# Optimization experiments

Hardware: AMD Instinct MI355X
Metric: run time of the kernel (lower is better)

## Reference

```python
import jax, jax.numpy as jnp
import numpy as np

N, E = 20000, 640000
F_IN, H, T = 64, 256, 64  # in_channels = T, edge_attr dim = T -> EdgeConv MLP in = 3*T


def _lin(key, fan_in, fan_out):
    k1, k2 = jax.random.split(key)
    s = 1.0 / np.sqrt(fan_in)
    W = jax.random.uniform(k1, (fan_in, fan_out), jnp.float32, -s, s)
    b = jax.random.uniform(k2, (fan_out,), jnp.float32, -s, s)
    return W, b


def setup_inputs() -> dict:
    key = jax.random.key(0)
    ks = jax.random.split(key, 12)
    x = jax.random.normal(ks[0], (N, F_IN), jnp.float32)
    edge_index = jax.random.randint(ks[1], (2, E), 0, N, jnp.int32)
    edge_attr = jax.random.normal(ks[2], (E, T), jnp.float32)
    conv1_W, conv1_b = _lin(ks[3], F_IN, H)
    e_W1, e_b1 = _lin(ks[4], 3 * T, H)
    e_W2, e_b2 = _lin(ks[5], H, H)
    conv2_W, conv2_b = _lin(ks[6], 2 * H, H)
    conv3_W, conv3_b = _lin(ks[7], H, F_IN)
    lin1_W, lin1_b = _lin(ks[8], 2 * F_IN, F_IN)
    lin2_W, lin2_b = _lin(ks[9], F_IN, 128)
    lin3_W, lin3_b = _lin(ks[10], 128, 32)
    lin4_W, lin4_b = _lin(ks[11], 32, 2)
    return dict(x=x, edge_index=edge_index, edge_attr=edge_attr,
                conv1_W=conv1_W, conv1_b=conv1_b,
                e_W1=e_W1, e_b1=e_b1, e_W2=e_W2, e_b2=e_b2,
                conv2_W=conv2_W, conv2_b=conv2_b,
                conv3_W=conv3_W, conv3_b=conv3_b,
                lin1_W=lin1_W, lin1_b=lin1_b, lin2_W=lin2_W, lin2_b=lin2_b,
                lin3_W=lin3_W, lin3_b=lin3_b, lin4_W=lin4_W, lin4_b=lin4_b)


def reference(x, edge_index, edge_attr,
              conv1_W, conv1_b, e_W1, e_b1, e_W2, e_b2,
              conv2_W, conv2_b, conv3_W, conv3_b,
              lin1_W, lin1_b, lin2_W, lin2_b, lin3_W, lin3_b, lin4_W, lin4_b):
    n = x.shape[0]
    src, dst = edge_index[0], edge_index[1]
    # GCN symmetric norm with self-loops (deg counted on dst, +1 for self-loop)
    deg = jax.ops.segment_sum(jnp.ones_like(src, jnp.float32), dst, num_segments=n) + 1.0
    dis = jax.lax.rsqrt(deg)

    def gcn(h, W, b):
        hw = h @ W
        msg = hw[src] * (dis[src] * dis[dst])[:, None]
        # self-loop contribution: norm = dis[i]^2
        return jax.ops.segment_sum(msg, dst, num_segments=n) + hw * (dis * dis)[:, None] + b

    out1 = jax.nn.relu(gcn(x, conv1_W, conv1_b))
    # EdgeConv: MLP(cat[x_i, x_j, edge_attr]) with max aggregation onto dst (x_i = target)
    m = jnp.concatenate([x[dst], x[src], edge_attr], axis=1)      # [E, 3T]
    m = jax.nn.relu(m @ e_W1 + e_b1) @ e_W2 + e_b2                 # [E, H]
    agg = jax.ops.segment_max(m, dst, num_segments=n)
    agg = jnp.where(jnp.isfinite(agg), agg, 0.0)                   # nodes with no in-edges
    out_e1 = jax.nn.relu(agg)

    out2 = jax.nn.relu(gcn(jnp.concatenate([out1, out_e1], axis=1), conv2_W, conv2_b))
    out3 = jax.nn.relu(gcn(out2, conv3_W, conv3_b))
    h = jnp.concatenate([x, out3], axis=1)
    h = jax.nn.softplus(h @ lin1_W + lin1_b)
    h = jax.nn.softplus(h @ lin2_W + lin2_b)
    h = jax.nn.softplus(h @ lin3_W + lin3_b)
    h = h @ lin4_W + lin4_b                                        # [N, 2]
    return (h[:, 0], h[:, 1])
```

## Files before the change

kernel.cpp:

```cpp
#include <hip/hip_runtime.h>
#include <stdint.h>

typedef __bf16 bf16x8 __attribute__((ext_vector_type(8)));
typedef float f32x4 __attribute__((ext_vector_type(4)));
typedef unsigned short u16x8 __attribute__((ext_vector_type(8)));
typedef unsigned long long ull_t;
typedef unsigned short ushort_t;

#define DEV __device__ __forceinline__

DEV unsigned short f2bf(float f) {
  __bf16 b = (__bf16)f;
  return __builtin_bit_cast(unsigned short, b);
}

DEV float bf2f(unsigned short b) { return __uint_as_float((unsigned int)b << 16); }

DEV f32x4 zero4() { f32x4 z = {0.f, 0.f, 0.f, 0.f}; return z; }

DEV float softplusf(float v) { return (v > 15.f) ? v : log1pf(expf(v)); }

__global__ void pack_weight(const float* __restrict__ W, unsigned short* __restrict__ P,
                            int K, int Ncols, int permk) {
  int idx = blockIdx.x * 256 + threadIdx.x;
  if (idx >= K * Ncols) return;
  int j = idx & 7;
  int lane = (idx >> 3) & 63;
  int rest = idx >> 9;
  int NT = Ncols >> 4;
  int nt = rest % NT;
  int kt = rest / NT;
  int k = kt * 32 + ((j >> 2) * 16) + ((lane >> 4) * 4) + (j & 3);
  if (permk) k = (k & ~63) | ((k & 3) << 4) | ((k >> 2) & 15);
  int col = nt * 16 + (lane & 15);
  P[idx] = f2bf(W[(size_t)k * Ncols + col]);
}

__global__ void k_deg(const int* __restrict__ dst, int* __restrict__ degi, int E) {
  int i = blockIdx.x * 256 + threadIdx.x;
  if (i < E) atomicAdd(&degi[dst[i]], 1);
}

__global__ void k_dis(const int* __restrict__ degi, float* __restrict__ dis, int n) {
  int i = blockIdx.x * 256 + threadIdx.x;
  if (i < n) dis[i] = rsqrtf((float)degi[i] + 1.0f);
}

__global__ __launch_bounds__(1024) void k_scan(const int* __restrict__ degi,
                                               int* __restrict__ ptr, int n) {
  __shared__ int part[1024];
  const int tid = threadIdx.x;
  const int chunk = (n + 1023) / 1024;
  const int b = tid * chunk;
  const int e2 = min(n, b + chunk);
  int s = 0;
  for (int i = b; i < e2; ++i) s += degi[i];
  part[tid] = s;
  __syncthreads();
  for (int off = 1; off < 1024; off <<= 1) {
    int val = (tid >= off) ? part[tid - off] : 0;
    __syncthreads();
    part[tid] += val;
    __syncthreads();
  }
  int run = (tid == 0) ? 0 : part[tid - 1];
  for (int i = b; i < e2; ++i) {
    ptr[i] = run;
    run += degi[i];
  }
  if (tid == 1023) ptr[n] = run;
}

__global__ void k_fill(const int* __restrict__ srcs, const int* __restrict__ dsts,
                       const int* __restrict__ ptr, const float* __restrict__ dis,
                       int* __restrict__ fillc,
                       int2* __restrict__ sc_s, int* __restrict__ dst_s,
                       int* __restrict__ perm_s, int E) {
  int e = blockIdx.x * 256 + threadIdx.x;
  if (e >= E) return;
  int d = dsts[e];
  int s = srcs[e];
  int pos = ptr[d] + atomicAdd(&fillc[d], 1);
  float c = dis[s] * dis[d];
  sc_s[pos] = make_int2(s, __float_as_int(c));
  dst_s[pos] = d;
  perm_s[pos] = e;
}

template <int COLS, bool FINALIZE, bool INBF16>
__global__ __launch_bounds__(256) void k_gather_agg(
    const void* __restrict__ featv, const int2* __restrict__ sc,
    const int* __restrict__ ptr, const float* __restrict__ dis,
    const void* __restrict__ hwv, const float* __restrict__ bias,
    float* __restrict__ out, int n) {
  constexpr int V = COLS / 64;
  const int v = blockIdx.x * 4 + (threadIdx.x >> 6);
  if (v >= n) return;
  const int lane = threadIdx.x & 63;
  const int beg = ptr[v], end = ptr[v + 1];

  auto loadrow = [&](int s, float* f) {
    if constexpr (INBF16) {
      const ushort_t* feat = (const ushort_t*)featv;
      if constexpr (V == 4) {
        ushort4 u = *(const ushort4*)(feat + (size_t)s * COLS + lane * 4);
        f[0] = bf2f(u.x); f[1] = bf2f(u.y); f[2] = bf2f(u.z); f[3] = bf2f(u.w);
      } else {
        f[0] = bf2f(feat[(size_t)s * COLS + lane]);
      }
    } else {
      const float* feat = (const float*)featv;
      if constexpr (V == 4) {
        float4 q = *(const float4*)(feat + (size_t)s * COLS + lane * 4);
        f[0] = q.x; f[1] = q.y; f[2] = q.z; f[3] = q.w;
      } else {
        f[0] = feat[(size_t)s * COLS + lane];
      }
    }
  };

  float acc[V];
#pragma unroll
  for (int i = 0; i < V; ++i) acc[i] = 0.f;
  const int cnt = end - beg;
  const int2* scp = sc + beg;
  int i = 0;
  for (; i + 4 <= cnt; i += 4) {
    int2 s0 = scp[i], s1 = scp[i + 1], s2 = scp[i + 2], s3 = scp[i + 3];
    float f0[V], f1[V], f2[V], f3[V];
    loadrow(s0.x, f0); loadrow(s1.x, f1); loadrow(s2.x, f2); loadrow(s3.x, f3);
    float c0 = __int_as_float(s0.y), c1 = __int_as_float(s1.y);
    float c2 = __int_as_float(s2.y), c3 = __int_as_float(s3.y);
#pragma unroll
    for (int j = 0; j < V; ++j)
      acc[j] += f0[j] * c0 + f1[j] * c1 + f2[j] * c2 + f3[j] * c3;
  }
  for (; i < cnt; ++i) {
    int2 s0 = scp[i];
    float c0 = __int_as_float(s0.y);
    float f0[V];
    loadrow(s0.x, f0);
#pragma unroll
    for (int j = 0; j < V; ++j) acc[j] += f0[j] * c0;
  }
  float* op = out + (size_t)v * COLS + lane * V;
  if constexpr (FINALIZE) {
    const float dv = dis[v];
    float d2 = dv * dv;
    float h[V];
    if constexpr (INBF16) {
      const ushort_t* hw = (const ushort_t*)hwv;
      if constexpr (V == 4) {
        ushort4 u = *(const ushort4*)(hw + (size_t)v * COLS + lane * 4);
        h[0] = bf2f(u.x); h[1] = bf2f(u.y); h[2] = bf2f(u.z); h[3] = bf2f(u.w);
      } else {
        h[0] = bf2f(hw[(size_t)v * COLS + lane]);
      }
    } else {
      const float* hw = (const float*)hwv;
      if constexpr (V == 4) {
        float4 q = *(const float4*)(hw + (size_t)v * COLS + lane * 4);
        h[0] = q.x; h[1] = q.y; h[2] = q.z; h[3] = q.w;
      } else {
        h[0] = hw[(size_t)v * COLS + lane];
      }
    }
#pragma unroll
    for (int i2 = 0; i2 < V; ++i2)
      acc[i2] = fmaxf(acc[i2] + h[i2] * d2 + bias[lane * V + i2], 0.f);
  }
  if constexpr (V == 4) {
    *(float4*)op = make_float4(acc[0], acc[1], acc[2], acc[3]);
  } else {
    op[0] = acc[0];
  }
}

template <int K, int NOUT, bool COMPOSE, bool RELUBIAS, bool OUTBF16>
__global__ __launch_bounds__(256, 2) void gcn_gemm(
    const float* __restrict__ inA, const float* __restrict__ inB,
    const float* __restrict__ dis,
    const unsigned short* __restrict__ Wp, const float* __restrict__ bias,
    void* __restrict__ outv, int out_stride, int nrows) {
  constexpr int NT = NOUT / 16;
  constexpr int NTW = NOUT / 64;
  __shared__ unsigned short s_in[64 * K];
  const int tid = threadIdx.x;
  const int r0 = blockIdx.x * 64;

  constexpr int C4R = K / 4;
  for (int idx = tid; idx < 64 * C4R; idx += 256) {
    int row = idx / C4R;
    int rem = idx - row * C4R;
    int grow = r0 + row;
    float4 v = make_float4(0.f, 0.f, 0.f, 0.f);
    if (grow < nrows) {
      v = *(const float4*)&inA[(size_t)grow * K + rem * 4];
      if constexpr (COMPOSE) {
        float d = dis[grow];
        d *= d;
        float4 w2 = *(const float4*)&inB[(size_t)grow * K + rem * 4];
        v.x += w2.x * d; v.y += w2.y * d; v.z += w2.z * d; v.w += w2.w * d;
      }
    }
    ushort4 b;
    b.x = f2bf(v.x); b.y = f2bf(v.y); b.z = f2bf(v.z); b.w = f2bf(v.w);
    *(ushort4*)&s_in[row * K + ((rem ^ (row & 7)) * 4)] = b;
  }
  __syncthreads();

  const int lane = tid & 63, wid = tid >> 6;
  const int lr = lane & 15, lg = lane >> 4;
  f32x4 acc[4][NTW];
#pragma unroll
  for (int m = 0; m < 4; ++m)
#pragma unroll
    for (int n2 = 0; n2 < NTW; ++n2) acc[m][n2] = zero4();

#pragma unroll
  for (int kt = 0; kt < K / 32; ++kt) {
    bf16x8 a[4];
#pragma unroll
    for (int m = 0; m < 4; ++m) {
      int rA = m * 16 + lr;
      int c1 = (kt * 8 + lg) ^ (rA & 7);
      int c2 = (kt * 8 + lg + 4) ^ (rA & 7);
      union { bf16x8 v; ull_t q[2]; } u;
      u.q[0] = *(const ull_t*)&s_in[rA * K + c1 * 4];
      u.q[1] = *(const ull_t*)&s_in[rA * K + c2 * 4];
      a[m] = u.v;
    }
#pragma unroll
    for (int n2 = 0; n2 < NTW; ++n2) {
      int nt = wid * NTW + n2;
      bf16x8 b = *(const bf16x8*)&Wp[(((kt * NT + nt) * 64 + lane) * 8)];
#pragma unroll
      for (int m = 0; m < 4; ++m)
        acc[m][n2] = __builtin_amdgcn_mfma_f32_16x16x32_bf16(a[m], b, acc[m][n2], 0, 0, 0);
    }
  }

#pragma unroll
  for (int n2 = 0; n2 < NTW; ++n2) {
    int col = (wid * NTW + n2) * 16 + lr;
    float bv = 0.f;
    if (RELUBIAS) bv = bias[col];
#pragma unroll
    for (int m = 0; m < 4; ++m) {
#pragma unroll
      for (int r = 0; r < 4; ++r) {
        int grow = r0 + m * 16 + lg * 4 + r;
        if (grow < nrows) {
          float v = acc[m][n2][r];
          if (RELUBIAS) v = fmaxf(v + bv, 0.f);
          if constexpr (OUTBF16) {
            ((ushort_t*)outv)[(size_t)grow * out_stride + col] = f2bf(v);
          } else {
            ((float*)outv)[(size_t)grow * out_stride + col] = v;
          }
        }
      }
    }
  }
}

__global__ __launch_bounds__(512, 4) void k_edgeconv(
    const float* __restrict__ x, const float* __restrict__ ea,
    const int2* __restrict__ sc_s, const int* __restrict__ dst_s,
    const int* __restrict__ perm_s,
    const unsigned short* __restrict__ W1p, const float* __restrict__ b1,
    const unsigned short* __restrict__ W2p, const float* __restrict__ b2,
    float* __restrict__ h2, int E) {
  __shared__ unsigned short s_buf[256 * 72];
  __shared__ int s_src[64], s_dst[64], s_perm[64];
  __shared__ ull_t s_mask;
  const int tid = threadIdx.x;
  const int e0 = blockIdx.x * 64;
  const int lane = tid & 63, wid = tid >> 6;
  if (tid < 64) {
    int e = e0 + tid;
    s_src[tid] = (e < E) ? sc_s[e].x : 0;
    s_dst[tid] = (e < E) ? dst_s[e] : 0;
    s_perm[tid] = (e < E) ? perm_s[e] : 0;
  }
  __syncthreads();
  if (wid == 0) {
    bool chg = (lane > 0) && (s_dst[lane] != s_dst[lane - 1]);
    ull_t m = __ballot(chg);
    if (lane == 0) s_mask = m;
  }
#pragma unroll
  for (int seg = 0; seg < 3; ++seg) {
#pragma unroll
    for (int it = 0; it < 2; ++it) {
      int idx = it * 512 + tid;
      int ei = idx >> 4;
      int q = idx & 15;
      const float* row;
      if (seg == 0) row = x + (unsigned)s_dst[ei] * 64u;
      else if (seg == 1) row = x + (unsigned)s_src[ei] * 64u;
      else row = ea + (unsigned)s_perm[ei] * 64u;
      float4 v = make_float4(0.f, 0.f, 0.f, 0.f);
      if (e0 + ei < E) v = *(const float4*)(row + q * 4);
      ushort4 b;
      b.x = f2bf(v.x); b.y = f2bf(v.y); b.z = f2bf(v.z); b.w = f2bf(v.w);
      int chunk = (seg * 16 + q) ^ (ei & 7);
      *(ushort4*)&s_buf[ei * 192 + chunk * 4] = b;
    }
  }

  const int wr = wid >> 2;
  const int wc = wid & 3;
  const int lr = lane & 15, lg = lane >> 4;

  bf16x8 bn1[4];
#pragma unroll
  for (int n2 = 0; n2 < 4; ++n2)
    bn1[n2] = *(const bf16x8*)&W1p[(((0 * 16 + wc * 4 + n2) * 64 + lane) * 8)];

  __syncthreads();

  f32x4 acc[2][4];
#pragma unroll
  for (int m = 0; m < 2; ++m)
#pragma unroll
    for (int n2 = 0; n2 < 4; ++n2) acc[m][n2] = zero4();

#pragma unroll
  for (int kt = 0; kt < 6; ++kt) {
    bf16x8 bc[4];
#pragma unroll
    for (int n2 = 0; n2 < 4; ++n2) bc[n2] = bn1[n2];
    if (kt < 5) {
#pragma unroll
      for (int n2 = 0; n2 < 4; ++n2)
        bn1[n2] = *(const bf16x8*)&W1p[((((kt + 1) * 16 + wc * 4 + n2) * 64 + lane) * 8)];
    }
    bf16x8 a[2];
#pragma unroll
    for (int m = 0; m < 2; ++m) {
      int rA = wr * 32 + m * 16 + lr;
      int rr = rA & 7;
      union { bf16x8 v; ull_t q[2]; } u;
      u.q[0] = *(const ull_t*)&s_buf[rA * 192 + ((kt * 8 + lg) ^ rr) * 4];
      u.q[1] = *(const ull_t*)&s_buf[rA * 192 + ((kt * 8 + lg + 4) ^ rr) * 4];
      a[m] = u.v;
    }
#pragma unroll
    for (int n2 = 0; n2 < 4; ++n2)
#pragma unroll
      for (int m = 0; m < 2; ++m)
        acc[m][n2] = __builtin_amdgcn_mfma_f32_16x16x32_bf16(a[m], bc[n2], acc[m][n2], 0, 0, 0);
  }

  bf16x8 bn2[4];
#pragma unroll
  for (int n2 = 0; n2 < 4; ++n2)
    bn2[n2] = *(const bf16x8*)&W2p[(((0 * 16 + wc * 4 + n2) * 64 + lane) * 8)];

  __syncthreads();

  {
    float b1v[4];
#pragma unroll
    for (int n2 = 0; n2 < 4; ++n2) b1v[n2] = b1[(wc * 4 + n2) * 16 + lr];
#pragma unroll
    for (int m = 0; m < 2; ++m) {
#pragma unroll
      for (int r = 0; r < 4; ++r) {
        int row = wr * 32 + m * 16 + lg * 4 + r;
        union { ushort_t h[4]; ull_t q; } pk;
        pk.h[0] = f2bf(fmaxf(acc[m][0][r] + b1v[0], 0.f));
        pk.h[1] = f2bf(fmaxf(acc[m][1][r] + b1v[1], 0.f));
        pk.h[2] = f2bf(fmaxf(acc[m][2][r] + b1v[2], 0.f));
        pk.h[3] = f2bf(fmaxf(acc[m][3][r] + b1v[3], 0.f));
        int chunk = (wc * 16 + lr) ^ (row & 7);
        *(ull_t*)&s_buf[row * 256 + chunk * 4] = pk.q;
      }
    }
  }
  __syncthreads();

#pragma unroll
  for (int m = 0; m < 2; ++m)
#pragma unroll
    for (int n2 = 0; n2 < 4; ++n2) acc[m][n2] = zero4();
#pragma unroll
  for (int kt = 0; kt < 8; ++kt) {
    bf16x8 bc[4];
#pragma unroll
    for (int n2 = 0; n2 < 4; ++n2) bc[n2] = bn2[n2];
    if (kt < 7) {
#pragma unroll
      for (int n2 = 0; n2 < 4; ++n2)
        bn2[n2] = *(const bf16x8*)&W2p[((((kt + 1) * 16 + wc * 4 + n2) * 64 + lane) * 8)];
    }
    bf16x8 a[2];
#pragma unroll
    for (int m = 0; m < 2; ++m) {
      int rA = wr * 32 + m * 16 + lr;
      int rr = rA & 7;
      union { bf16x8 v; ull_t q[2]; } u;
      u.q[0] = *(const ull_t*)&s_buf[rA * 256 + ((kt * 8 + lg) ^ rr) * 4];
      u.q[1] = *(const ull_t*)&s_buf[rA * 256 + ((kt * 8 + lg + 4) ^ rr) * 4];
      a[m] = u.v;
    }
#pragma unroll
    for (int n2 = 0; n2 < 4; ++n2)
#pragma unroll
      for (int m = 0; m < 2; ++m)
        acc[m][n2] = __builtin_amdgcn_mfma_f32_16x16x32_bf16(a[m], bc[n2], acc[m][n2], 0, 0, 0);
  }
  __syncthreads();

#pragma unroll
  for (int n2 = 0; n2 < 4; ++n2) {
    int col = (wc * 4 + n2) * 16 + lr;
    float bv = b2[col];
#pragma unroll
    for (int m = 0; m < 2; ++m) {
      int rbase = wr * 32 + m * 16 + lg * 4;
      union { ushort_t h[4]; ull_t q; } pk;
#pragma unroll
      for (int r = 0; r < 4; ++r) {
        int row = rbase + r;
        float v = (e0 + row < E) ? fmaxf(acc[m][n2][r] + bv, 0.f) : 0.f;
        pk.h[r] = f2bf(v);
      }
      *(ull_t*)&s_buf[col * 72 + rbase] = pk.q;
    }
  }
  __syncthreads();

  {
    const int col = tid & 255;
    const int half = tid >> 8;
    const int rbeg = half * 32;
    const unsigned int mask = (unsigned int)(s_mask >> rbeg);
    unsigned int run = 0;
    int segstart = rbeg;
#pragma unroll
    for (int i = 0; i < 4; ++i) {
      u16x8 pack = *(const u16x8*)&s_buf[col * 72 + rbeg + i * 8];
#pragma unroll
      for (int r2 = 0; r2 < 8; ++r2) {
        int rloc = i * 8 + r2;
        if (mask & (1u << rloc)) {
          if (run > 0)
            atomicMax((int*)h2 + ((unsigned)s_dst[segstart] * 512u + 256u + col),
                      (int)(run << 16));
          run = 0;
          segstart = rbeg + rloc;
        }
        run = max(run, (unsigned int)pack[r2]);
      }
    }
    if (run > 0)
      atomicMax((int*)h2 + ((unsigned)s_dst[segstart] * 512u + 256u + col),
                (int)(run << 16));
  }
}

__global__ __launch_bounds__(256) void k_head(
    const float* __restrict__ x, const float* __restrict__ out3,
    const float* __restrict__ W1, const float* __restrict__ b1,
    const float* __restrict__ W2, const float* __restrict__ b2,
    const float* __restrict__ W3, const float* __restrict__ b3,
    const float* __restrict__ W4, const float* __restrict__ b4,
    float* __restrict__ out, int n) {
  __shared__ float sW1[128 * 64];
  __shared__ float sW3[128 * 32];
  __shared__ float sW4[32 * 2];
  __shared__ float sb1[64], sb2[128], sb3[32], sb4[2];
  __shared__ float sbuf[4][352];
  const int tid = threadIdx.x;
  for (int i = tid; i < 128 * 64; i += 256) sW1[i] = W1[i];
  for (int i = tid; i < 128 * 32; i += 256) sW3[i] = W3[i];
  if (tid < 64) sW4[tid] = W4[tid];
  if (tid < 64) sb1[tid] = b1[tid];
  if (tid < 128) sb2[tid] = b2[tid];
  if (tid < 32) sb3[tid] = b3[tid];
  if (tid < 2) sb4[tid] = b4[tid];
  __syncthreads();
  const int wid = tid >> 6, lane = tid & 63;
  float* B = sbuf[wid];
  const int per = gridDim.x * 4;
  const int iters = (n + per - 1) / per;
  for (int it = 0; it < iters; ++it) {
    const int node = it * per + blockIdx.x * 4 + wid;
    const bool act = node < n;
    if (act) {
      B[lane] = x[(size_t)node * 64 + lane];
      B[64 + lane] = out3[(size_t)node * 64 + lane];
    }
    __syncthreads();
    if (act) {
      float o = sb1[lane];
#pragma unroll 8
      for (int k = 0; k < 128; ++k) o += B[k] * sW1[k * 64 + lane];
      B[128 + lane] = softplusf(o);
    }
    __syncthreads();
    if (act) {
      float o0 = sb2[lane], o1 = sb2[64 + lane];
#pragma unroll 8
      for (int k = 0; k < 64; ++k) {
        float v = B[128 + k];
        o0 += v * W2[k * 128 + lane];
        o1 += v * W2[k * 128 + 64 + lane];
      }
      B[192 + lane] = softplusf(o0);
      B[256 + lane] = softplusf(o1);
    }
    __syncthreads();
    if (act && lane < 32) {
      float o = sb3[lane];
#pragma unroll 8
      for (int k = 0; k < 128; ++k) o += B[192 + k] * sW3[k * 32 + lane];
      B[320 + lane] = softplusf(o);
    }
    __syncthreads();
    if (act && lane < 2) {
      float o = sb4[lane];
#pragma unroll
      for (int k = 0; k < 32; ++k) o += B[320 + k] * sW4[k * 2 + lane];
      out[(size_t)lane * n + node] = o;
    }
    __syncthreads();
  }
}

static inline size_t alignup(size_t v) { return (v + 255) & ~(size_t)255; }

extern "C" void kernel_launch(void* const* d_in, const int* in_sizes, int n_in,
                              void* d_out, int out_size, void* d_ws, size_t ws_size,
                              hipStream_t stream) {
  const float* x = (const float*)d_in[0];
  const int* ei = (const int*)d_in[1];
  const float* ea = (const float*)d_in[2];
  const float* c1W = (const float*)d_in[3];
  const float* c1b = (const float*)d_in[4];
  const float* eW1 = (const float*)d_in[5];
  const float* eb1 = (const float*)d_in[6];
  const float* eW2 = (const float*)d_in[7];
  const float* eb2 = (const float*)d_in[8];
  const float* c2W = (const float*)d_in[9];
  const float* c2b = (const float*)d_in[10];
  const float* c3W = (const float*)d_in[11];
  const float* c3b = (const float*)d_in[12];
  const float* l1W = (const float*)d_in[13];
  const float* l1b = (const float*)d_in[14];
  const float* l2W = (const float*)d_in[15];
  const float* l2b = (const float*)d_in[16];
  const float* l3W = (const float*)d_in[17];
  const float* l3b = (const float*)d_in[18];
  const float* l4W = (const float*)d_in[19];
  const float* l4b = (const float*)d_in[20];
  const int n = in_sizes[0] / 64;
  const int E = in_sizes[1] / 2;
  const int* srcs = ei;
  const int* dsts = ei + E;

  char* w = (char*)d_ws;
  auto alloc = [&](size_t bytes) {
    char* p = w;
    w += alignup(bytes);
    return p;
  };
  float* dis = (float*)alloc((size_t)n * 4);
  int* degi = (int*)alloc((size_t)n * 4);
  int* ptr = (int*)alloc((size_t)(n + 1) * 4);
  int* fillc = (int*)alloc((size_t)n * 4);
  int2* sc_s = (int2*)alloc((size_t)E * 8);
  int* dst_s = (int*)alloc((size_t)E * 4);
  int* perm_s = (int*)alloc((size_t)E * 4);
  float* agg1 = (float*)alloc((size_t)n * 64 * 4);
  float* h2 = (float*)alloc((size_t)n * 512 * 4);
  ushort_t* hw2b = (ushort_t*)alloc((size_t)n * 256 * 2);
  float* out2 = (float*)alloc((size_t)n * 256 * 4);
  ushort_t* hw3b = (ushort_t*)alloc((size_t)n * 64 * 2);
  float* out3 = (float*)alloc((size_t)n * 64 * 4);
  unsigned short* p_c1 = (unsigned short*)alloc(64 * 256 * 2);
  unsigned short* p_e1 = (unsigned short*)alloc(192 * 256 * 2);
  unsigned short* p_e2 = (unsigned short*)alloc(256 * 256 * 2);
  unsigned short* p_c2 = (unsigned short*)alloc(512 * 256 * 2);
  unsigned short* p_c3 = (unsigned short*)alloc(256 * 64 * 2);

  hipMemsetAsync(degi, 0, (size_t)n * 4, stream);
  hipMemsetAsync(fillc, 0, (size_t)n * 4, stream);
  hipMemsetAsync(h2, 0, (size_t)n * 512 * 4, stream);

  pack_weight<<<(64 * 256) / 256, 256, 0, stream>>>(c1W, p_c1, 64, 256, 0);
  pack_weight<<<(192 * 256) / 256, 256, 0, stream>>>(eW1, p_e1, 192, 256, 0);
  pack_weight<<<(256 * 256) / 256, 256, 0, stream>>>(eW2, p_e2, 256, 256, 1);
  pack_weight<<<(512 * 256) / 256, 256, 0, stream>>>(c2W, p_c2, 512, 256, 0);
  pack_weight<<<(256 * 64) / 256, 256, 0, stream>>>(c3W, p_c3, 256, 64, 0);

  k_deg<<<(E + 255) / 256, 256, 0, stream>>>(dsts, degi, E);
  k_dis<<<(n + 255) / 256, 256, 0, stream>>>(degi, dis, n);
  k_scan<<<1, 1024, 0, stream>>>(degi, ptr, n);
  k_fill<<<(E + 255) / 256, 256, 0, stream>>>(srcs, dsts, ptr, dis, fillc,
                                              sc_s, dst_s, perm_s, E);

  const int ablocks = (n + 3) / 4;
  const int gblocks = (n + 63) / 64;

  k_gather_agg<64, false, false><<<ablocks, 256, 0, stream>>>(
      x, sc_s, ptr, dis, nullptr, nullptr, agg1, n);
  gcn_gemm<64, 256, true, true, false><<<gblocks, 256, 0, stream>>>(
      agg1, x, dis, p_c1, c1b, h2, 512, n);

  k_edgeconv<<<(E + 63) / 64, 512, 0, stream>>>(x, ea, sc_s, dst_s, perm_s,
                                                p_e1, eb1, p_e2, eb2, h2, E);

  gcn_gemm<512, 256, false, false, true><<<gblocks, 256, 0, stream>>>(
      h2, nullptr, nullptr, p_c2, nullptr, hw2b, 256, n);
  k_gather_agg<256, true, true><<<ablocks, 256, 0, stream>>>(
      hw2b, sc_s, ptr, dis, hw2b, c2b, out2, n);

  gcn_gemm<256, 64, false, false, true><<<gblocks, 256, 0, stream>>>(
      out2, nullptr, nullptr, p_c3, nullptr, hw3b, 64, n);
  k_gather_agg<64, true, true><<<ablocks, 256, 0, stream>>>(
      hw3b, sc_s, ptr, dis, hw3b, c3b, out3, n);

  k_head<<<1250, 256, 0, stream>>>(x, out3, l1W, l1b, l2W, l2b, l3W, l3b, l4W, l4b,
                                   (float*)d_out, n);
}
```

Before: 599.5 us.

## Double edge tile per EdgeConv block and gather conv1 input from bf16 x

The EdgeConv kernel now handles 128 edges per block instead of 64. Each wave computes 4 row tiles, so every weight fragment loaded from global memory feeds twice as many MFMAs, and the software prefetch of weights is dropped. Shared memory grows to about 70KB and accumulator registers double, which may reduce occupancy under the 512-thread launch bounds. Separately, x is converted once to bf16 so the first GCN aggregation gathers half as many bytes, at the cost of an extra conversion kernel and bf16 rounding of the aggregated input.

```diff
diff --git a/kernel.cpp b/kernel.cpp
--- a/kernel.cpp
+++ b/kernel.cpp
@@ -36,6 +36,16 @@
   P[idx] = f2bf(W[(size_t)k * Ncols + col]);
 }
 
+__global__ void k_cvt_bf16(const float* __restrict__ in, ushort_t* __restrict__ out,
+                           int n4) {
+  int i = blockIdx.x * 256 + threadIdx.x;
+  if (i >= n4) return;
+  float4 v = *(const float4*)(in + (size_t)i * 4);
+  ushort4 b;
+  b.x = f2bf(v.x); b.y = f2bf(v.y); b.z = f2bf(v.z); b.w = f2bf(v.w);
+  *(ushort4*)(out + (size_t)i * 4) = b;
+}
+
 __global__ void k_deg(const int* __restrict__ dst, int* __restrict__ degi, int E) {
   int i = blockIdx.x * 256 + threadIdx.x;
   if (i < E) atomicAdd(&degi[dst[i]], 1);
@@ -271,28 +281,29 @@
     const unsigned short* __restrict__ W1p, const float* __restrict__ b1,
     const unsigned short* __restrict__ W2p, const float* __restrict__ b2,
     float* __restrict__ h2, int E) {
-  __shared__ unsigned short s_buf[256 * 72];
-  __shared__ int s_src[64], s_dst[64], s_perm[64];
-  __shared__ ull_t s_mask;
+  __shared__ unsigned short s_buf[256 * 136];
+  __shared__ int s_src[128], s_dst[128], s_perm[128];
+  __shared__ ull_t s_mask[2];
   const int tid = threadIdx.x;
-  const int e0 = blockIdx.x * 64;
+  const int e0 = blockIdx.x * 128;
   const int lane = tid & 63, wid = tid >> 6;
-  if (tid < 64) {
+  if (tid < 128) {
     int e = e0 + tid;
     s_src[tid] = (e < E) ? sc_s[e].x : 0;
     s_dst[tid] = (e < E) ? dst_s[e] : 0;
     s_perm[tid] = (e < E) ? perm_s[e] : 0;
   }
   __syncthreads();
-  if (wid == 0) {
-    bool chg = (lane > 0) && (s_dst[lane] != s_dst[lane - 1]);
+  if (wid < 2) {
+    int r = wid * 64 + lane;
+    bool chg = (r > 0) && (s_dst[r] != s_dst[r - 1]);
     ull_t m = __ballot(chg);
-    if (lane == 0) s_mask = m;
+    if (lane == 0) s_mask[wid] = m;
   }
 #pragma unroll
   for (int seg = 0; seg < 3; ++seg) {
 #pragma unroll
-    for (int it = 0; it < 2; ++it) {
+    for (int it = 0; it < 4; ++it) {
       int idx = it * 512 + tid;
       int ei = idx >> 4;
       int q = idx & 15;
@@ -308,38 +319,23 @@
       *(ushort4*)&s_buf[ei * 192 + chunk * 4] = b;
     }
   }
+  __syncthreads();
 
   const int wr = wid >> 2;
   const int wc = wid & 3;
   const int lr = lane & 15, lg = lane >> 4;
-
-  bf16x8 bn1[4];
-#pragma unroll
-  for (int n2 = 0; n2 < 4; ++n2)
-    bn1[n2] = *(const bf16x8*)&W1p[(((0 * 16 + wc * 4 + n2) * 64 + lane) * 8)];
-
-  __syncthreads();
-
-  f32x4 acc[2][4];
-#pragma unroll
-  for (int m = 0; m < 2; ++m)
+  f32x4 acc[4][4];
+#pragma unroll
+  for (int m = 0; m < 4; ++m)
 #pragma unroll
     for (int n2 = 0; n2 < 4; ++n2) acc[m][n2] = zero4();
 
 #pragma unroll
   for (int kt = 0; kt < 6; ++kt) {
-    bf16x8 bc[4];
-#pragma unroll
-    for (int n2 = 0; n2 < 4; ++n2) bc[n2] = bn1[n2];
-    if (kt < 5) {
-#pragma unroll
-      for (int n2 = 0; n2 < 4; ++n2)
-        bn1[n2] = *(const bf16x8*)&W1p[((((kt + 1) * 16 + wc * 4 + n2) * 64 + lane) * 8)];
-    }
-    bf16x8 a[2];
-#pragma unroll
-    for (int m = 0; m < 2; ++m) {
-      int rA = wr * 32 + m * 16 + lr;
+    bf16x8 a[4];
+#pragma unroll
+    for (int m = 0; m < 4; ++m) {
+      int rA = wr * 64 + m * 16 + lr;
       int rr = rA & 7;
       union { bf16x8 v; ull_t q[2]; } u;
       u.q[0] = *(const ull_t*)&s_buf[rA * 192 + ((kt * 8 + lg) ^ rr) * 4];
@@ -347,17 +343,14 @@
       a[m] = u.v;
     }
 #pragma unroll
-    for (int n2 = 0; n2 < 4; ++n2)
-#pragma unroll
-      for (int m = 0; m < 2; ++m)
-        acc[m][n2] = __builtin_amdgcn_mfma_f32_16x16x32_bf16(a[m], bc[n2], acc[m][n2], 0, 0, 0);
-  }
-
-  bf16x8 bn2[4];
-#pragma unroll
-  for (int n2 = 0; n2 < 4; ++n2)
-    bn2[n2] = *(const bf16x8*)&W2p[(((0 * 16 + wc * 4 + n2) * 64 + lane) * 8)];
-
+    for (int n2 = 0; n2 < 4; ++n2) {
+      int nt = wc * 4 + n2;
+      bf16x8 b = *(const bf16x8*)&W1p[(((kt * 16 + nt) * 64 + lane) * 8)];
+#pragma unroll
+      for (int m = 0; m < 4; ++m)
+        acc[m][n2] = __builtin_amdgcn_mfma_f32_16x16x32_bf16(a[m], b, acc[m][n2], 0, 0, 0);
+    }
+  }
   __syncthreads();
 
   {
@@ -365,10 +358,10 @@
 #pragma unroll
     for (int n2 = 0; n2 < 4; ++n2) b1v[n2] = b1[(wc * 4 + n2) * 16 + lr];
 #pragma unroll
-    for (int m = 0; m < 2; ++m) {
+    for (int m = 0; m < 4; ++m) {
 #pragma unroll
       for (int r = 0; r < 4; ++r) {
-        int row = wr * 32 + m * 16 + lg * 4 + r;
+        int row = wr * 64 + m * 16 + lg * 4 + r;
         union { ushort_t h[4]; ull_t q; } pk;
         pk.h[0] = f2bf(fmaxf(acc[m][0][r] + b1v[0], 0.f));
         pk.h[1] = f2bf(fmaxf(acc[m][1][r] + b1v[1], 0.f));
@@ -382,23 +375,15 @@
   __syncthreads();
 
 #pragma unroll
-  for (int m = 0; m < 2; ++m)
+  for (int m = 0; m < 4; ++m)
 #pragma unroll
     for (int n2 = 0; n2 < 4; ++n2) acc[m][n2] = zero4();
 #pragma unroll
   for (int kt = 0; kt < 8; ++kt) {
-    bf16x8 bc[4];
-#pragma unroll
-    for (int n2 = 0; n2 < 4; ++n2) bc[n2] = bn2[n2];
-    if (kt < 7) {
-#pragma unroll
-      for (int n2 = 0; n2 < 4; ++n2)
-        bn2[n2] = *(const bf16x8*)&W2p[((((kt + 1) * 16 + wc * 4 + n2) * 64 + lane) * 8)];
-    }
-    bf16x8 a[2];
-#pragma unroll
-    for (int m = 0; m < 2; ++m) {
-      int rA = wr * 32 + m * 16 + lr;
+    bf16x8 a[4];
+#pragma unroll
+    for (int m = 0; m < 4; ++m) {
+      int rA = wr * 64 + m * 16 + lr;
       int rr = rA & 7;
       union { bf16x8 v; ull_t q[2]; } u;
       u.q[0] = *(const ull_t*)&s_buf[rA * 256 + ((kt * 8 + lg) ^ rr) * 4];
@@ -406,10 +391,13 @@
       a[m] = u.v;
     }
 #pragma unroll
-    for (int n2 = 0; n2 < 4; ++n2)
-#pragma unroll
-      for (int m = 0; m < 2; ++m)
-        acc[m][n2] = __builtin_amdgcn_mfma_f32_16x16x32_bf16(a[m], bc[n2], acc[m][n2], 0, 0, 0);
+    for (int n2 = 0; n2 < 4; ++n2) {
+      int nt = wc * 4 + n2;
+      bf16x8 b = *(const bf16x8*)&W2p[(((kt * 16 + nt) * 64 + lane) * 8)];
+#pragma unroll
+      for (int m = 0; m < 4; ++m)
+        acc[m][n2] = __builtin_amdgcn_mfma_f32_16x16x32_bf16(a[m], b, acc[m][n2], 0, 0, 0);
+    }
   }
   __syncthreads();
 
@@ -418,8 +406,8 @@
     int col = (wc * 4 + n2) * 16 + lr;
     float bv = b2[col];
 #pragma unroll
-    for (int m = 0; m < 2; ++m) {
-      int rbase = wr * 32 + m * 16 + lg * 4;
+    for (int m = 0; m < 4; ++m) {
+      int rbase = wr * 64 + m * 16 + lg * 4;
       union { ushort_t h[4]; ull_t q; } pk;
 #pragma unroll
       for (int r = 0; r < 4; ++r) {
@@ -427,7 +415,7 @@
         float v = (e0 + row < E) ? fmaxf(acc[m][n2][r] + bv, 0.f) : 0.f;
         pk.h[r] = f2bf(v);
       }
-      *(ull_t*)&s_buf[col * 72 + rbase] = pk.q;
+      *(ull_t*)&s_buf[col * 136 + rbase] = pk.q;
     }
   }
   __syncthreads();
@@ -435,17 +423,17 @@
   {
     const int col = tid & 255;
     const int half = tid >> 8;
-    const int rbeg = half * 32;
-    const unsigned int mask = (unsigned int)(s_mask >> rbeg);
+    const int rbeg = half * 64;
+    const ull_t mask = s_mask[half];
     unsigned int run = 0;
     int segstart = rbeg;
 #pragma unroll
-    for (int i = 0; i < 4; ++i) {
-      u16x8 pack = *(const u16x8*)&s_buf[col * 72 + rbeg + i * 8];
+    for (int i = 0; i < 8; ++i) {
+      u16x8 pack = *(const u16x8*)&s_buf[col * 136 + rbeg + i * 8];
 #pragma unroll
       for (int r2 = 0; r2 < 8; ++r2) {
         int rloc = i * 8 + r2;
-        if (mask & (1u << rloc)) {
+        if ((mask >> rloc) & 1ull) {
           if (run > 0)
             atomicMax((int*)h2 + ((unsigned)s_dst[segstart] * 512u + 256u + col),
                       (int)(run << 16));
@@ -580,6 +568,7 @@
   float* out2 = (float*)alloc((size_t)n * 256 * 4);
   ushort_t* hw3b = (ushort_t*)alloc((size_t)n * 64 * 2);
   float* out3 = (float*)alloc((size_t)n * 64 * 4);
+  ushort_t* xb = (ushort_t*)alloc((size_t)n * 64 * 2);
   unsigned short* p_c1 = (unsigned short*)alloc(64 * 256 * 2);
   unsigned short* p_e1 = (unsigned short*)alloc(192 * 256 * 2);
   unsigned short* p_e2 = (unsigned short*)alloc(256 * 256 * 2);
@@ -595,6 +584,7 @@
   pack_weight<<<(256 * 256) / 256, 256, 0, stream>>>(eW2, p_e2, 256, 256, 1);
   pack_weight<<<(512 * 256) / 256, 256, 0, stream>>>(c2W, p_c2, 512, 256, 0);
   pack_weight<<<(256 * 64) / 256, 256, 0, stream>>>(c3W, p_c3, 256, 64, 0);
+  k_cvt_bf16<<<(n * 16 + 255) / 256, 256, 0, stream>>>(x, xb, n * 16);
 
   k_deg<<<(E + 255) / 256, 256, 0, stream>>>(dsts, degi, E);
   k_dis<<<(n + 255) / 256, 256, 0, stream>>>(degi, dis, n);
@@ -605,13 +595,13 @@
   const int ablocks = (n + 3) / 4;
   const int gblocks = (n + 63) / 64;
 
-  k_gather_agg<64, false, false><<<ablocks, 256, 0, stream>>>(
-      x, sc_s, ptr, dis, nullptr, nullptr, agg1, n);
+  k_gather_agg<64, false, true><<<ablocks, 256, 0, stream>>>(
+      xb, sc_s, ptr, dis, nullptr, nullptr, agg1, n);
   gcn_gemm<64, 256, true, true, false><<<gblocks, 256, 0, stream>>>(
       agg1, x, dis, p_c1, c1b, h2, 512, n);
 
-  k_edgeconv<<<(E + 63) / 64, 512, 0, stream>>>(x, ea, sc_s, dst_s, perm_s,
-                                                p_e1, eb1, p_e2, eb2, h2, E);
+  k_edgeconv<<<(E + 127) / 128, 512, 0, stream>>>(x, ea, sc_s, dst_s, perm_s,
+                                                  p_e1, eb1, p_e2, eb2, h2, E);
 
   gcn_gemm<512, 256, false, false, true><<<gblocks, 256, 0, stream>>>(
       h2, nullptr, nullptr, p_c2, nullptr, hw2b, 256, n);
```

Result: no change. 599.8 us (+0.0%).
